# Kernel optimization log

Hardware: AMD Instinct MI355X
Metric: run time of the kernel (lower is better)

The kernel has to match this reference:

```python
import jax, jax.numpy as jnp
import numpy as np

N = 100000
E = 1280000
C = 64
MID = 256
OUT = 64
BN_EPS = 1e-5


def setup_inputs() -> dict:
    key = jax.random.key(0)
    ks = jax.random.split(key, 8)
    x = jax.random.normal(ks[0], (N, C), dtype=jnp.float32)
    edge_index = jax.random.randint(ks[1], (2, E), 0, N, dtype=jnp.int64)
    edge_attr = jax.random.normal(ks[2], (E, 1), dtype=jnp.float32)
    batch = jnp.zeros((N,), dtype=jnp.int64)
    # MLP params: Lin(2C->MID), BatchNorm1d(MID), Lin(MID->OUT)
    W1 = jax.random.normal(ks[3], (2 * C, MID), dtype=jnp.float32) / np.sqrt(2 * C)
    b1 = jnp.zeros((MID,), dtype=jnp.float32)
    gamma = jnp.ones((MID,), dtype=jnp.float32)
    beta = jnp.zeros((MID,), dtype=jnp.float32)
    W2 = jax.random.normal(ks[4], (MID, OUT), dtype=jnp.float32) / np.sqrt(MID)
    b2 = jnp.zeros((OUT,), dtype=jnp.float32)
    return {"x": x, "edge_index": edge_index, "edge_attr": edge_attr, "batch": batch,
            "W1": W1, "b1": b1, "gamma": gamma, "beta": beta, "W2": W2, "b2": b2}


def reference(x, edge_index, edge_attr, batch, W1, b1, gamma, beta, W2, b2):
    n = x.shape[0]
    row, col = edge_index[0], edge_index[1]
    xc = x[col]                                  # [E, C] irregular gather
    feat = jnp.concatenate([xc, xc * edge_attr], axis=1)  # [E, 2C]
    sums = jax.ops.segment_sum(feat, row, num_segments=n)  # [N, 2C]
    cnt = jax.ops.segment_sum(jnp.ones((feat.shape[0],), feat.dtype), row, num_segments=n)
    agg = sums / jnp.maximum(cnt, 1.0)[:, None]  # scatter_mean
    # MLP: Lin -> ReLU -> BatchNorm1d (training stats) -> Lin
    h = jax.nn.relu(agg @ W1 + b1)
    mu = jnp.mean(h, axis=0)
    var = jnp.var(h, axis=0)                     # biased var, as torch BN uses
    h = (h - mu) * jax.lax.rsqrt(var + BN_EPS) * gamma + beta
    return h @ W2 + b2
```

## Files before the change

### kernel.cpp

```cpp
#include <hip/hip_runtime.h>
#include <hip/hip_bf16.h>

#define MIDF 256
#define OUTF 64
#define CF 64
#define TWO_C 128
#define BN_EPS 1e-5f
#define BCAP 1024
#define NBMAX 1600

typedef __attribute__((ext_vector_type(8))) short bf16x8;
typedef __attribute__((ext_vector_type(4))) float f32x4;

__device__ __forceinline__ ushort f2bf(float f) {
  union { float f; unsigned u; } v; v.f = f;
  return (ushort)((v.u + 0x7fffu + ((v.u >> 16) & 1u)) >> 16);
}
__device__ __forceinline__ float bf2f(unsigned u16) {
  union { unsigned u; float f; } v; v.u = u16 << 16;
  return v.f;
}

__global__ __launch_bounds__(256) void k_xcast(const float4* __restrict__ xp,
    uint4* __restrict__ xb, int* __restrict__ gcur, float* __restrict__ bnacc,
    int n8, int NB) {
  int i = blockIdx.x * blockDim.x + threadIdx.x;
  if (i < NB) gcur[i] = i * BCAP;
  else if (i < NB + 512) bnacc[i - NB] = 0.f;
  int st = gridDim.x * blockDim.x;
  for (; i < n8; i += st) {
    float4 a = xp[2 * i], b = xp[2 * i + 1];
    uint4 o;
    o.x = (unsigned)f2bf(a.x) | ((unsigned)f2bf(a.y) << 16);
    o.y = (unsigned)f2bf(a.z) | ((unsigned)f2bf(a.w) << 16);
    o.z = (unsigned)f2bf(b.x) | ((unsigned)f2bf(b.y) << 16);
    o.w = (unsigned)f2bf(b.z) | ((unsigned)f2bf(b.w) << 16);
    xb[i] = o;
  }
}

__global__ __launch_bounds__(256) void k_bscatter(const int* __restrict__ ei,
    const float* __restrict__ ea, int* __restrict__ gcur,
    uint2* __restrict__ ebt, int E, int NB) {
  __shared__ int lh[NBMAX];
  __shared__ int lb[NBMAX];
  int tid = threadIdx.x;
  int c0 = blockIdx.x * 4096;
  for (int b = tid; b < NB; b += 256) lh[b] = 0;
  __syncthreads();
  int rows[16];
#pragma unroll
  for (int j = 0; j < 16; ++j) {
    int e = c0 + j * 256 + tid;
    int r = (e < E) ? ei[e] : -1;
    rows[j] = r;
    if (r >= 0) atomicAdd(&lh[r >> 6], 1);
  }
  __syncthreads();
  for (int b = tid; b < NB; b += 256) {
    int c = lh[b];
    lb[b] = (c > 0) ? atomicAdd(&gcur[b], c) : 0;
  }
  __syncthreads();
#pragma unroll
  for (int j = 0; j < 16; ++j) {
    int r = rows[j];
    if (r >= 0) {
      int e = c0 + j * 256 + tid;
      int pos = atomicAdd(&lb[r >> 6], 1);
      ebt[pos] = make_uint2((unsigned)ei[E + e] | ((unsigned)(r & 63) << 20),
                            __float_as_uint(ea[e]));
    }
  }
}

__global__ __launch_bounds__(512, 4) void k_sortagg(const ushort* __restrict__ xb,
    const uint2* __restrict__ ebt, const int* __restrict__ gcur,
    ushort* __restrict__ agg, int n) {
  __shared__ uint2 recs[BCAP];
  __shared__ int hist[64], cbase[64], cursor[64];
  int tid = threadIdx.x;
  int b = blockIdx.x;
  int base = b * BCAP;
  int cnt = gcur[b] - base;
  if (tid < 64) hist[tid] = 0;
  __syncthreads();
  for (int i = tid; i < cnt; i += 512)
    atomicAdd(&hist[(ebt[base + i].x >> 20) & 63], 1);
  __syncthreads();
  if (tid < 64) {
    int v = hist[tid];
    int sc = v;
#pragma unroll
    for (int d = 1; d < 64; d <<= 1) {
      int t = __shfl_up(sc, d);
      if (tid >= d) sc += t;
    }
    cbase[tid] = sc - v;
    cursor[tid] = sc - v;
  }
  __syncthreads();
  for (int i = tid; i < cnt; i += 512) {
    uint2 rec = ebt[base + i];
    int pos = atomicAdd(&cursor[(rec.x >> 20) & 63], 1);
    recs[pos] = make_uint2(rec.x & 0xFFFFF, rec.y);
  }
  __syncthreads();
  int w = tid >> 6, lane = tid & 63;
  int q4 = lane >> 4, l16 = lane & 15;
#pragma unroll
  for (int j = 0; j < 8; ++j) {
    int rl = w * 8 + j;
    int v = (b << 6) + rl;
    if (v >= n) continue;
    int s = cbase[rl], d = hist[rl];
    int e = s + d;
    float s0 = 0.f, s1 = 0.f, s2 = 0.f, s3 = 0.f;
    float t0 = 0.f, t1 = 0.f, t2 = 0.f, t3 = 0.f;
    int i = s + q4;
    for (; i + 4 < e; i += 8) {
      uint2 pa = recs[i], pb = recs[i + 4];
      uint2 xa = *(const uint2*)(xb + (size_t)pa.x * CF + 4 * l16);
      uint2 xc = *(const uint2*)(xb + (size_t)pb.x * CF + 4 * l16);
      float wa = __uint_as_float(pa.y), wb = __uint_as_float(pb.y);
      float a0 = bf2f(xa.x & 0xffff), a1 = bf2f(xa.x >> 16);
      float a2 = bf2f(xa.y & 0xffff), a3 = bf2f(xa.y >> 16);
      float b0 = bf2f(xc.x & 0xffff), b1 = bf2f(xc.x >> 16);
      float b2 = bf2f(xc.y & 0xffff), b3 = bf2f(xc.y >> 16);
      s0 += a0 + b0; s1 += a1 + b1; s2 += a2 + b2; s3 += a3 + b3;
      t0 += a0 * wa + b0 * wb; t1 += a1 * wa + b1 * wb;
      t2 += a2 * wa + b2 * wb; t3 += a3 * wa + b3 * wb;
    }
    if (i < e) {
      uint2 p = recs[i];
      uint2 xv = *(const uint2*)(xb + (size_t)p.x * CF + 4 * l16);
      float wt = __uint_as_float(p.y);
      float a0 = bf2f(xv.x & 0xffff), a1 = bf2f(xv.x >> 16);
      float a2 = bf2f(xv.y & 0xffff), a3 = bf2f(xv.y >> 16);
      s0 += a0; s1 += a1; s2 += a2; s3 += a3;
      t0 += a0 * wt; t1 += a1 * wt; t2 += a2 * wt; t3 += a3 * wt;
    }
    s0 += __shfl_xor(s0, 16); s1 += __shfl_xor(s1, 16);
    s2 += __shfl_xor(s2, 16); s3 += __shfl_xor(s3, 16);
    t0 += __shfl_xor(t0, 16); t1 += __shfl_xor(t1, 16);
    t2 += __shfl_xor(t2, 16); t3 += __shfl_xor(t3, 16);
    s0 += __shfl_xor(s0, 32); s1 += __shfl_xor(s1, 32);
    s2 += __shfl_xor(s2, 32); s3 += __shfl_xor(s3, 32);
    t0 += __shfl_xor(t0, 32); t1 += __shfl_xor(t1, 32);
    t2 += __shfl_xor(t2, 32); t3 += __shfl_xor(t3, 32);
    float inv = 1.0f / fmaxf((float)d, 1.0f);
    if (q4 == 0) {
      uint2 o;
      o.x = (unsigned)f2bf(s0 * inv) | ((unsigned)f2bf(s1 * inv) << 16);
      o.y = (unsigned)f2bf(s2 * inv) | ((unsigned)f2bf(s3 * inv) << 16);
      *(uint2*)(agg + (size_t)v * TWO_C + 4 * l16) = o;
      uint2 p2;
      p2.x = (unsigned)f2bf(t0 * inv) | ((unsigned)f2bf(t1 * inv) << 16);
      p2.y = (unsigned)f2bf(t2 * inv) | ((unsigned)f2bf(t3 * inv) << 16);
      *(uint2*)(agg + (size_t)v * TWO_C + CF + 4 * l16) = p2;
    }
  }
}

__global__ __launch_bounds__(256, 3) void k_gemm1(const ushort* __restrict__ agg,
    const float* __restrict__ W1, const float* __restrict__ b1,
    ushort* __restrict__ h, float* __restrict__ bnacc, int n, int ntiles) {
  int tid = threadIdx.x, w = tid >> 6, lane = tid & 63;
  int q = lane >> 4, l16 = lane & 15;
  int cg = blockIdx.x & 3;
  int colbase = cg * 64;
  bf16x8 Bf[4][4];
#pragma unroll
  for (int ct = 0; ct < 4; ++ct)
#pragma unroll
    for (int ks = 0; ks < 4; ++ks) {
      int c = colbase + ct * 16 + l16;
      int k0 = ks * 32 + q * 8;
#pragma unroll
      for (int j = 0; j < 8; ++j)
        Bf[ct][ks][j] = (short)f2bf(W1[(size_t)(k0 + j) * MIDF + c]);
    }
  float bias[4];
#pragma unroll
  for (int ct = 0; ct < 4; ++ct) bias[ct] = b1[colbase + ct * 16 + l16];
  __shared__ ushort tile[64 * 72];
  int c_stat = tid & 63, rb = tid >> 6;
  float s_sum = 0.f, s_sq = 0.f;
  int nb = gridDim.x >> 2;
  for (int t = blockIdx.x >> 2; t < ntiles; t += nb) {
    int r0 = t * 64;
    int myrow = r0 + w * 16 + l16;
    bf16x8 Af[4];
#pragma unroll
    for (int ks = 0; ks < 4; ++ks) {
      bf16x8 av;
#pragma unroll
      for (int j = 0; j < 8; ++j) av[j] = 0;
      if (myrow < n) av = *(const bf16x8*)(agg + (size_t)myrow * TWO_C + ks * 32 + q * 8);
      Af[ks] = av;
    }
    f32x4 acc[4];
#pragma unroll
    for (int ct = 0; ct < 4; ++ct) acc[ct] = (f32x4){0.f, 0.f, 0.f, 0.f};
#pragma unroll
    for (int ks = 0; ks < 4; ++ks)
#pragma unroll
      for (int ct = 0; ct < 4; ++ct)
        acc[ct] = __builtin_amdgcn_mfma_f32_16x16x32_bf16(Af[ks], Bf[ct][ks], acc[ct], 0, 0, 0);
    __syncthreads();
#pragma unroll
    for (int ct = 0; ct < 4; ++ct)
#pragma unroll
      for (int r = 0; r < 4; ++r) {
        float vv = fmaxf(acc[ct][r] + bias[ct], 0.f);
        tile[(w * 16 + q * 4 + r) * 72 + ct * 16 + l16] = f2bf(vv);
      }
    __syncthreads();
    int row = tid >> 2, co = (tid & 3) * 16;
    int gr = r0 + row;
    if (gr < n) {
      const uint4* src = (const uint4*)(tile + row * 72 + co);
      uint4* dst = (uint4*)(h + (size_t)gr * MIDF + colbase + co);
      dst[0] = src[0];
      dst[1] = src[1];
    }
#pragma unroll 4
    for (int r = 0; r < 16; ++r) {
      int rr = rb * 16 + r;
      if (r0 + rr < n) {
        float vv = bf2f(tile[rr * 72 + c_stat]);
        s_sum += vv;
        s_sq += vv * vv;
      }
    }
  }
  __syncthreads();
  float* red = (float*)tile;
  red[rb * 64 + c_stat] = s_sum;
  red[256 + rb * 64 + c_stat] = s_sq;
  __syncthreads();
  if (tid < 128) {
    int c = tid & 63, isq = tid >> 6;
    int base = isq * 256;
    float v = red[base + c] + red[base + 64 + c] + red[base + 128 + c] + red[base + 192 + c];
    atomicAdd(&bnacc[isq * MIDF + colbase + c], v);
  }
}

__global__ __launch_bounds__(256) void k_final(const float* __restrict__ bnacc,
    const float* __restrict__ gamma, const float* __restrict__ beta,
    const float* __restrict__ W2, const float* __restrict__ b2,
    float* __restrict__ W2p, float* __restrict__ b2p, float invN) {
  __shared__ float scb[MIDF], shb[MIDF], red[256];
  int tid = threadIdx.x;
  float s = bnacc[tid];
  float q = bnacc[MIDF + tid];
  float mu = s * invN;
  float var = q * invN - mu * mu;
  float sc = gamma[tid] * rsqrtf(var + BN_EPS);
  scb[tid] = sc;
  shb[tid] = beta[tid] - mu * sc;
  __syncthreads();
  float sp = 0.f;
  for (int i = tid; i < MIDF * OUTF; i += 256) {
    int k = i >> 6;
    float wv = W2[i];
    W2p[i] = scb[k] * wv;
    sp += shb[k] * wv;
  }
  red[tid] = sp;
  __syncthreads();
  if (tid < 64)
    b2p[tid] = b2[tid] + red[tid] + red[64 + tid] + red[128 + tid] + red[192 + tid];
}

__global__ __launch_bounds__(256, 2) void k_gemm2(const ushort* __restrict__ h,
    const float* __restrict__ W2p, const float* __restrict__ b2p,
    float* __restrict__ out, int n, int ntiles) {
  int tid = threadIdx.x, w = tid >> 6, lane = tid & 63;
  int q = lane >> 4, l16 = lane & 15;
  bf16x8 Bf[4][8];
#pragma unroll
  for (int ct = 0; ct < 4; ++ct)
#pragma unroll
    for (int ks = 0; ks < 8; ++ks) {
      int c = ct * 16 + l16;
      int k0 = ks * 32 + q * 8;
#pragma unroll
      for (int j = 0; j < 8; ++j)
        Bf[ct][ks][j] = (short)f2bf(W2p[(size_t)(k0 + j) * OUTF + c]);
    }
  float bias[4];
#pragma unroll
  for (int ct = 0; ct < 4; ++ct) bias[ct] = b2p[ct * 16 + l16];
  __shared__ float tile[64 * 68];
  for (int t = blockIdx.x; t < ntiles; t += gridDim.x) {
    int r0 = t * 64;
    int myrow = r0 + w * 16 + l16;
    f32x4 acc[4];
#pragma unroll
    for (int ct = 0; ct < 4; ++ct) acc[ct] = (f32x4){0.f, 0.f, 0.f, 0.f};
#pragma unroll
    for (int ks = 0; ks < 8; ++ks) {
      bf16x8 av;
#pragma unroll
      for (int j = 0; j < 8; ++j) av[j] = 0;
      if (myrow < n) av = *(const bf16x8*)(h + (size_t)myrow * MIDF + ks * 32 + q * 8);
#pragma unroll
      for (int ct = 0; ct < 4; ++ct)
        acc[ct] = __builtin_amdgcn_mfma_f32_16x16x32_bf16(av, Bf[ct][ks], acc[ct], 0, 0, 0);
    }
    __syncthreads();
#pragma unroll
    for (int ct = 0; ct < 4; ++ct)
#pragma unroll
      for (int r = 0; r < 4; ++r)
        tile[(w * 16 + q * 4 + r) * 68 + ct * 16 + l16] = acc[ct][r] + bias[ct];
    __syncthreads();
    int row = tid >> 2, co = (tid & 3) * 16;
    int gr = r0 + row;
    if (gr < n) {
      const float4* src = (const float4*)(tile + row * 68 + co);
      float4* dst = (float4*)(out + (size_t)gr * OUTF + co);
      dst[0] = src[0];
      dst[1] = src[1];
      dst[2] = src[2];
      dst[3] = src[3];
    }
  }
}

extern "C" void kernel_launch(void* const* d_in, const int* in_sizes, int n_in,
                              void* d_out, int out_size, void* d_ws, size_t ws_size,
                              hipStream_t stream) {
  const float* x     = (const float*)d_in[0];
  const int*   ei    = (const int*)d_in[1];
  const float* ea    = (const float*)d_in[2];
  const float* W1    = (const float*)d_in[4];
  const float* b1    = (const float*)d_in[5];
  const float* gamma = (const float*)d_in[6];
  const float* beta  = (const float*)d_in[7];
  const float* W2    = (const float*)d_in[8];
  const float* b2    = (const float*)d_in[9];
  float* out = (float*)d_out;
  int E = in_sizes[2];
  int n = in_sizes[3];
  int NB = (n + 63) >> 6;

  char* ws = (char*)d_ws;
  ushort* agg = (ushort*)ws;
  ushort* h   = agg + (size_t)n * TWO_C;
  ushort* xb  = h + (size_t)n * MIDF;
  float* W2p  = (float*)(xb + (size_t)n * CF);
  float* b2p  = W2p + MIDF * OUTF;
  int* gcur   = (int*)(b2p + 64);
  float* bnacc= (float*)(gcur + NBMAX);
  uint2* ebt  = (uint2*)h;

  hipLaunchKernelGGL(k_xcast, dim3(512), dim3(256), 0, stream,
                     (const float4*)x, (uint4*)xb, gcur, bnacc, n * CF / 8, NB);
  int nchunks = (E + 4095) / 4096;
  hipLaunchKernelGGL(k_bscatter, dim3(nchunks), dim3(256), 0, stream, ei, ea, gcur, ebt, E, NB);
  hipLaunchKernelGGL(k_sortagg, dim3(NB), dim3(512), 0, stream, xb, ebt, gcur, agg, n);
  int nt = (n + 63) / 64;
  hipLaunchKernelGGL(k_gemm1, dim3(768), dim3(256), 0, stream, agg, W1, b1, h, bnacc, n, nt);
  hipLaunchKernelGGL(k_final, dim3(1), dim3(256), 0, stream, bnacc, gamma, beta,
                     W2, b2, W2p, b2p, 1.0f / (float)n);
  hipLaunchKernelGGL(k_gemm2, dim3(512), dim3(256), 0, stream, h, W2p, b2p, out, n, nt);
}
```

Before: 243.9 us.

## Run x bf16 cast concurrently with edge bucket scatter in one kernel

Splits the x-to-bf16 cast out of the init kernel and fuses it into the edge bucketing kernel as extra blocks, so the cast and the scatter run at the same time. A tiny single-block kernel now does the cursor and BN accumulator initialisation. The bucketing blocks grow to 1024 threads with 4 edges per thread instead of 256 threads with 16. This removes one serial dependency between launches, at the cost of larger blocks with more LDS-atomic contention per block and possibly lower occupancy.

Result: faster. 238.1 us (-2.4%).

```diff
diff --git a/kernel.cpp b/kernel.cpp
--- a/kernel.cpp
+++ b/kernel.cpp
@@ -21,52 +21,58 @@
   return v.f;
 }
 
-__global__ __launch_bounds__(256) void k_xcast(const float4* __restrict__ xp,
-    uint4* __restrict__ xb, int* __restrict__ gcur, float* __restrict__ bnacc,
-    int n8, int NB) {
-  int i = blockIdx.x * blockDim.x + threadIdx.x;
-  if (i < NB) gcur[i] = i * BCAP;
-  else if (i < NB + 512) bnacc[i - NB] = 0.f;
-  int st = gridDim.x * blockDim.x;
-  for (; i < n8; i += st) {
-    float4 a = xp[2 * i], b = xp[2 * i + 1];
-    uint4 o;
-    o.x = (unsigned)f2bf(a.x) | ((unsigned)f2bf(a.y) << 16);
-    o.y = (unsigned)f2bf(a.z) | ((unsigned)f2bf(a.w) << 16);
-    o.z = (unsigned)f2bf(b.x) | ((unsigned)f2bf(b.y) << 16);
-    o.w = (unsigned)f2bf(b.z) | ((unsigned)f2bf(b.w) << 16);
-    xb[i] = o;
-  }
-}
-
-__global__ __launch_bounds__(256) void k_bscatter(const int* __restrict__ ei,
-    const float* __restrict__ ea, int* __restrict__ gcur,
-    uint2* __restrict__ ebt, int E, int NB) {
+__global__ __launch_bounds__(1024) void k_init(int* __restrict__ gcur,
+                                               float* __restrict__ bnacc, int NB) {
+  int i = threadIdx.x;
+  for (; i < NB; i += 1024) gcur[i] = i * BCAP;
+  i = threadIdx.x;
+  if (i < 512) bnacc[i] = 0.f;
+}
+
+__global__ __launch_bounds__(1024) void k_front(const int* __restrict__ ei,
+    const float* __restrict__ ea, int* __restrict__ gcur, uint2* __restrict__ ebt,
+    int E, int NB, int nchunks,
+    const float4* __restrict__ xp, uint4* __restrict__ xb, int n8) {
   __shared__ int lh[NBMAX];
   __shared__ int lb[NBMAX];
   int tid = threadIdx.x;
+  if ((int)blockIdx.x >= nchunks) {
+    int nb2 = gridDim.x - nchunks;
+    int i = ((int)blockIdx.x - nchunks) * 1024 + tid;
+    int st = nb2 * 1024;
+    for (; i < n8; i += st) {
+      float4 a = xp[2 * i], b = xp[2 * i + 1];
+      uint4 o;
+      o.x = (unsigned)f2bf(a.x) | ((unsigned)f2bf(a.y) << 16);
+      o.y = (unsigned)f2bf(a.z) | ((unsigned)f2bf(a.w) << 16);
+      o.z = (unsigned)f2bf(b.x) | ((unsigned)f2bf(b.y) << 16);
+      o.w = (unsigned)f2bf(b.z) | ((unsigned)f2bf(b.w) << 16);
+      xb[i] = o;
+    }
+    return;
+  }
   int c0 = blockIdx.x * 4096;
-  for (int b = tid; b < NB; b += 256) lh[b] = 0;
-  __syncthreads();
-  int rows[16];
-#pragma unroll
-  for (int j = 0; j < 16; ++j) {
-    int e = c0 + j * 256 + tid;
+  for (int b = tid; b < NB; b += 1024) lh[b] = 0;
+  __syncthreads();
+  int rows[4];
+#pragma unroll
+  for (int j = 0; j < 4; ++j) {
+    int e = c0 + j * 1024 + tid;
     int r = (e < E) ? ei[e] : -1;
     rows[j] = r;
     if (r >= 0) atomicAdd(&lh[r >> 6], 1);
   }
   __syncthreads();
-  for (int b = tid; b < NB; b += 256) {
+  for (int b = tid; b < NB; b += 1024) {
     int c = lh[b];
     lb[b] = (c > 0) ? atomicAdd(&gcur[b], c) : 0;
   }
   __syncthreads();
 #pragma unroll
-  for (int j = 0; j < 16; ++j) {
+  for (int j = 0; j < 4; ++j) {
     int r = rows[j];
     if (r >= 0) {
-      int e = c0 + j * 256 + tid;
+      int e = c0 + j * 1024 + tid;
       int pos = atomicAdd(&lb[r >> 6], 1);
       ebt[pos] = make_uint2((unsigned)ei[E + e] | ((unsigned)(r & 63) << 20),
                             __float_as_uint(ea[e]));
@@ -357,10 +363,11 @@
   float* bnacc= (float*)(gcur + NBMAX);
   uint2* ebt  = (uint2*)h;
 
-  hipLaunchKernelGGL(k_xcast, dim3(512), dim3(256), 0, stream,
-                     (const float4*)x, (uint4*)xb, gcur, bnacc, n * CF / 8, NB);
   int nchunks = (E + 4095) / 4096;
-  hipLaunchKernelGGL(k_bscatter, dim3(nchunks), dim3(256), 0, stream, ei, ea, gcur, ebt, E, NB);
+  hipLaunchKernelGGL(k_init, dim3(1), dim3(1024), 0, stream, gcur, bnacc, NB);
+  hipLaunchKernelGGL(k_front, dim3(nchunks + 256), dim3(1024), 0, stream,
+                     ei, ea, gcur, ebt, E, NB, nchunks,
+                     (const float4*)x, (uint4*)xb, n * CF / 8);
   hipLaunchKernelGGL(k_sortagg, dim3(NB), dim3(512), 0, stream, xb, ebt, gcur, agg, n);
   int nt = (n + 63) / 64;
   hipLaunchKernelGGL(k_gemm1, dim3(768), dim3(256), 0, stream, agg, W1, b1, h, bnacc, n, nt);
```
